# Kernel optimization log

Measured on AMD Instinct MI355X. Metric: run time of the kernel, lower is better.

## Reference

```python
import jax, jax.numpy as jnp
import numpy as np

B, N, M = 2, 1024, 512
D, H, DH = 1024, 16, 64          # features, heads, head dim (D == H*DH)
MID = H * DH
DC = 768                          # context_features
MULT = 4
EPS = 1e-5


def _ln(x, w, b):
    mu = jnp.mean(x, -1, keepdims=True)
    var = jnp.mean((x - mu) ** 2, -1, keepdims=True)
    return (x - mu) * jax.lax.rsqrt(var + EPS) * w + b


def _sincos(n, d):
    inv = 1.0 / (10000.0 ** (jnp.arange(0, d, 2, dtype=jnp.float32) / d))
    ang = jnp.arange(n, dtype=jnp.float32)[:, None] * inv[None, :]
    return jnp.sin(ang), jnp.cos(ang)


def _rope(x, sin, cos):
    # x: [B,H,N,DH]; sin/cos: [N, DH//2]; interleaved even/odd rotation
    s = sin[None, None]
    c = cos[None, None]
    xe = x[..., ::2]
    xo = x[..., 1::2]
    re = xe * c - xo * s
    ro = xe * s + xo * c
    return jnp.stack((re, ro), axis=-1).reshape(x.shape)


def _heads(t):
    b, n, _ = t.shape
    return t.reshape(b, n, H, DH).transpose(0, 2, 1, 3)


def _attn(xq, ctx, wq, wkv, wo, bo):
    q = _heads(xq @ wq)
    k, v = jnp.split(ctx @ wkv, 2, axis=-1)
    k = _heads(k)
    v = _heads(v)
    sq, cq = _sincos(q.shape[2], DH)
    sk, ck = _sincos(k.shape[2], DH)
    q = _rope(q, sq, cq)
    k = _rope(k, sk, ck)
    sim = jnp.einsum('bhnd,bhmd->bhnm', q, k) * (DH ** -0.5)
    a = jax.nn.softmax(sim, axis=-1)
    o = jnp.einsum('bhnm,bhmd->bhnd', a, v)
    o = o.transpose(0, 2, 1, 3).reshape(xq.shape[0], xq.shape[1], MID)
    return o @ wo + bo


def _adaln(x, c, lw, lb, gw, gb, bw, bb):
    g = (c @ gw + gb)[:, None, :]
    bt = (c @ bw + bb)[:, None, :]
    return _ln(x, lw, lb) * (1.0 + g) + bt


def setup_inputs() -> dict:
    ks = jax.random.split(jax.random.key(0), 24)
    s = 0.02
    inp = {
        'x': jax.random.normal(ks[0], (B, N, D), jnp.float32),
        'cond': jax.random.normal(ks[1], (B, D), jnp.float32),
        'context': jax.random.normal(ks[2], (B, M, DC), jnp.float32),
        # AdaLN (attn_mod) — reused for self- and cross-attention pre-norm
        'ln1_w': jnp.ones((D,), jnp.float32),
        'ln1_b': jnp.zeros((D,), jnp.float32),
        'g1_w': jax.random.normal(ks[3], (D, D), jnp.float32) * s,
        'g1_b': jnp.zeros((D,), jnp.float32),
        'b1_w': jax.random.normal(ks[4], (D, D), jnp.float32) * s,
        'b1_b': jnp.zeros((D,), jnp.float32),
        # AdaLN (ffn_mod)
        'ln2_w': jnp.ones((D,), jnp.float32),
        'ln2_b': jnp.zeros((D,), jnp.float32),
        'g2_w': jax.random.normal(ks[5], (D, D), jnp.float32) * s,
        'g2_b': jnp.zeros((D,), jnp.float32),
        'b2_w': jax.random.normal(ks[6], (D, D), jnp.float32) * s,
        'b2_b': jnp.zeros((D,), jnp.float32),
        # self-attention
        'sa_wq': jax.random.normal(ks[7], (D, MID), jnp.float32) * s,
        'sa_wkv': jax.random.normal(ks[8], (D, 2 * MID), jnp.float32) * s,
        'sa_wo': jax.random.normal(ks[9], (MID, D), jnp.float32) * s,
        'sa_bo': jnp.zeros((D,), jnp.float32),
        # cross-attention (context LayerNorm + projections)
        'ca_lnc_w': jnp.ones((DC,), jnp.float32),
        'ca_lnc_b': jnp.zeros((DC,), jnp.float32),
        'ca_wq': jax.random.normal(ks[10], (D, MID), jnp.float32) * s,
        'ca_wkv': jax.random.normal(ks[11], (DC, 2 * MID), jnp.float32) * s,
        'ca_wo': jax.random.normal(ks[12], (MID, D), jnp.float32) * s,
        'ca_bo': jnp.zeros((D,), jnp.float32),
        # FFN
        'ff_w1': jax.random.normal(ks[13], (D, MULT * D), jnp.float32) * s,
        'ff_b1': jnp.zeros((MULT * D,), jnp.float32),
        'ff_w2': jax.random.normal(ks[14], (MULT * D, D), jnp.float32) * s,
        'ff_b2': jnp.zeros((D,), jnp.float32),
    }
    return inp


def reference(x, cond, context,
              ln1_w, ln1_b, g1_w, g1_b, b1_w, b1_b,
              ln2_w, ln2_b, g2_w, g2_b, b2_w, b2_b,
              sa_wq, sa_wkv, sa_wo, sa_bo,
              ca_lnc_w, ca_lnc_b, ca_wq, ca_wkv, ca_wo, ca_bo,
              ff_w1, ff_b1, ff_w2, ff_b2):
    # self-attention with shared attn_mod AdaLN
    attn_in = _adaln(x, cond, ln1_w, ln1_b, g1_w, g1_b, b1_w, b1_b)
    x = _attn(attn_in, attn_in, sa_wq, sa_wkv, sa_wo, sa_bo) + x
    # cross-attention (attn_mod reused, context LayerNorm applied)
    cross_in = _adaln(x, cond, ln1_w, ln1_b, g1_w, g1_b, b1_w, b1_b)
    ctx_n = _ln(context, ca_lnc_w, ca_lnc_b)
    x = _attn(cross_in, ctx_n, ca_wq, ca_wkv, ca_wo, ca_bo) + x
    # FFN with ffn_mod AdaLN, exact GELU (torch default)
    ffn_in = _adaln(x, cond, ln2_w, ln2_b, g2_w, g2_b, b2_w, b2_b)
    h = jax.nn.gelu(ffn_in @ ff_w1 + ff_b1, approximate=False)
    x = h @ ff_w2 + ff_b2 + x
    return x
```

## Files before the change

kernel.cpp:

```cpp
#include <hip/hip_runtime.h>
#include <hip/hip_bf16.h>
#include <math.h>


typedef float f32x4 __attribute__((ext_vector_type(4)));
typedef __bf16 bf16x8 __attribute__((ext_vector_type(8)));
typedef __bf16 bf16x4 __attribute__((ext_vector_type(4)));
typedef __bf16 bf16x2 __attribute__((ext_vector_type(2)));

#define DEVI __device__ __forceinline__

DEVI void gload16(const void* g, void* l) {
  __builtin_amdgcn_global_load_lds((const __attribute__((address_space(1))) void*)g,
                                   (__attribute__((address_space(3))) void*)l, 16, 0, 0);
}

DEVI float fast_gelu(float x) {
  float a = fabsf(x) * 0.7071067811865475f;
  float tt = 1.0f / (1.0f + 0.3275911f * a);
  float p = tt * (0.254829592f + tt * (-0.284496736f + tt * (1.421413741f +
            tt * (-1.453152027f + tt * 1.061405429f))));
  float er = 1.0f - p * __expf(-a * a);
  er = (x < 0.f) ? -er : er;
  return 0.5f * x * (1.0f + er);
}

struct WtDesc {
  const float* src[8];
  __bf16* dst[8];
  int K[8], N[8];
  int tstart[9];
};

__global__ __launch_bounds__(256) void prep_kernel(WtDesc d,
                                                   float2* __restrict__ tbl,
                                                   const float* __restrict__ cond,
                                                   const float* __restrict__ g1w,
                                                   const float* __restrict__ b1w,
                                                   const float* __restrict__ g2w,
                                                   const float* __restrict__ b2w,
                                                   float* __restrict__ part) {
  __shared__ float smem[32 * 129];
  int blk = blockIdx.x;
  int wtend = d.tstart[8];
  int t = threadIdx.x;
  if (blk < wtend) {
    int e = 0;
#pragma unroll
    for (int i = 0; i < 7; ++i) e += (blk >= d.tstart[i + 1]) ? 1 : 0;
    int li = blk - d.tstart[e];
    const float* W = d.src[e];
    __bf16* WT = d.dst[e];
    int K = d.K[e], N = d.N[e];
    int ntx = N >> 7;
    int n0 = (li % ntx) * 128, k0 = (li / ntx) * 32;
    int tx = t & 31, ty = t >> 5;
#pragma unroll
    for (int i = 0; i < 4; ++i) {
      int k = ty + i * 8;
      f32x4 v = *(const f32x4*)(W + (size_t)(k0 + k) * N + n0 + tx * 4);
#pragma unroll
      for (int j = 0; j < 4; ++j) smem[k * 129 + tx * 4 + j] = v[j];
    }
    __syncthreads();
    int kc = t & 3;
#pragma unroll
    for (int i = 0; i < 2; ++i) {
      int n = i * 64 + (t >> 2);
      bf16x8 o;
#pragma unroll
      for (int j = 0; j < 8; ++j) o[j] = (__bf16)smem[(kc * 8 + j) * 129 + n];
      *(bf16x8*)(WT + (size_t)(n0 + n) * K + k0 + kc * 8) = o;
    }
  } else if (blk < wtend + 128) {
    int idx = (blk - wtend) * 256 + t;
    int n = idx >> 5, i = idx & 31;
    float inv = expf(-(float)(2 * i) * (1.0f / 64.0f) * 9.210340371976184f);
    float ang = (float)n * inv;
    tbl[idx] = make_float2(sinf(ang), cosf(ang));
  } else {
    int f = blk - wtend - 128;
    int dchunk = f & 3, b = (f >> 2) & 1, z = f >> 3;
    int mat = z >> 3, ks = z & 7;
    const float* W = (mat == 0) ? g1w : (mat == 1) ? b1w : (mat == 2) ? g2w : b2w;
    float* sc = smem;
    if (t < 128) sc[t] = cond[b * 1024 + ks * 128 + t];
    __syncthreads();
    int dd = dchunk * 256 + t;
    const float* Wp = W + (size_t)(ks * 128) * 1024 + dd;
    float acc = 0.f;
#pragma unroll 8
    for (int k = 0; k < 128; ++k) acc += sc[k] * Wp[(size_t)k * 1024];
    part[(size_t)(z * 2 + b) * 1024 + dd] = acc;
  }
}

__global__ __launch_bounds__(256) void mod_reduce_kernel(
    const float* __restrict__ part,
    const float* __restrict__ g1b, const float* __restrict__ b1b,
    const float* __restrict__ g2b, const float* __restrict__ b2b,
    float* __restrict__ mods) {
  int idx = blockIdx.x * 256 + threadIdx.x;
  int mat = idx >> 11, b = (idx >> 10) & 1, d = idx & 1023;
  float s = 0.f;
#pragma unroll
  for (int ks = 0; ks < 8; ++ks) s += part[(size_t)((mat * 8 + ks) * 2 + b) * 1024 + d];
  const float* Bv = (mat == 0) ? g1b : (mat == 1) ? b1b : (mat == 2) ? g2b : b2b;
  mods[(size_t)(mat * 2 + b) * 1024 + d] = s + Bv[d];
}

__global__ __launch_bounds__(256) void adaln_kernel(const float* __restrict__ X,
                                                    const float* __restrict__ lnw,
                                                    const float* __restrict__ lnb,
                                                    const float* __restrict__ mods,
                                                    int gi, int bi,
                                                    __bf16* __restrict__ out) {
  __shared__ float red[2][4];
  int row = blockIdx.x;
  int b = row >> 10;
  int t = threadIdx.x;
  const float4 xv = ((const float4*)(X + (size_t)row * 1024))[t];
  float s  = xv.x + xv.y + xv.z + xv.w;
  float s2 = xv.x * xv.x + xv.y * xv.y + xv.z * xv.z + xv.w * xv.w;
  int lane = t & 63, w = t >> 6;
#pragma unroll
  for (int off = 32; off > 0; off >>= 1) {
    s += __shfl_down(s, off);
    s2 += __shfl_down(s2, off);
  }
  if (lane == 0) { red[0][w] = s; red[1][w] = s2; }
  __syncthreads();
  s  = red[0][0] + red[0][1] + red[0][2] + red[0][3];
  s2 = red[1][0] + red[1][1] + red[1][2] + red[1][3];
  float mu = s * (1.0f / 1024.0f);
  float var = s2 * (1.0f / 1024.0f) - mu * mu;
  float rstd = rsqrtf(var + 1e-5f);
  const float4 wv = ((const float4*)lnw)[t];
  const float4 bv = ((const float4*)lnb)[t];
  const float4 gv = ((const float4*)(mods + (size_t)(gi * 2 + b) * 1024))[t];
  const float4 tv = ((const float4*)(mods + (size_t)(bi * 2 + b) * 1024))[t];
  bf16x4 ov;
  ov[0] = (__bf16)(((xv.x - mu) * rstd * wv.x + bv.x) * (1.0f + gv.x) + tv.x);
  ov[1] = (__bf16)(((xv.y - mu) * rstd * wv.y + bv.y) * (1.0f + gv.y) + tv.y);
  ov[2] = (__bf16)(((xv.z - mu) * rstd * wv.z + bv.z) * (1.0f + gv.z) + tv.z);
  ov[3] = (__bf16)(((xv.w - mu) * rstd * wv.w + bv.w) * (1.0f + gv.w) + tv.w);
  *(bf16x4*)(out + (size_t)row * 1024 + t * 4) = ov;
}

__global__ __launch_bounds__(256) void red_adaln_kernel(const float* __restrict__ part,
                                                        const float* __restrict__ bias,
                                                        const float* __restrict__ res,
                                                        const float* __restrict__ lnw,
                                                        const float* __restrict__ lnb,
                                                        const float* __restrict__ mods,
                                                        int gi, int bi, int MN,
                                                        float* __restrict__ xout,
                                                        __bf16* __restrict__ ain) {
  __shared__ float red[2][4];
  int row = blockIdx.x;
  int b = row >> 10;
  int t = threadIdx.x;
  size_t base = (size_t)row * 1024 + t * 4;
  float4 p0 = *(const float4*)(part + base);
  float4 p1 = *(const float4*)(part + MN + base);
  float4 rr = *(const float4*)(res + base);
  float4 bb = ((const float4*)bias)[t];
  float4 y;
  y.x = p0.x + p1.x + bb.x + rr.x;
  y.y = p0.y + p1.y + bb.y + rr.y;
  y.z = p0.z + p1.z + bb.z + rr.z;
  y.w = p0.w + p1.w + bb.w + rr.w;
  *(float4*)(xout + base) = y;
  float s  = y.x + y.y + y.z + y.w;
  float s2 = y.x * y.x + y.y * y.y + y.z * y.z + y.w * y.w;
  int lane = t & 63, w = t >> 6;
#pragma unroll
  for (int off = 32; off > 0; off >>= 1) {
    s += __shfl_down(s, off);
    s2 += __shfl_down(s2, off);
  }
  if (lane == 0) { red[0][w] = s; red[1][w] = s2; }
  __syncthreads();
  s  = red[0][0] + red[0][1] + red[0][2] + red[0][3];
  s2 = red[1][0] + red[1][1] + red[1][2] + red[1][3];
  float mu = s * (1.0f / 1024.0f);
  float var = s2 * (1.0f / 1024.0f) - mu * mu;
  float rstd = rsqrtf(var + 1e-5f);
  const float4 wv = ((const float4*)lnw)[t];
  const float4 bv = ((const float4*)lnb)[t];
  const float4 gv = ((const float4*)(mods + (size_t)(gi * 2 + b) * 1024))[t];
  const float4 tv = ((const float4*)(mods + (size_t)(bi * 2 + b) * 1024))[t];
  bf16x4 ov;
  ov[0] = (__bf16)(((y.x - mu) * rstd * wv.x + bv.x) * (1.0f + gv.x) + tv.x);
  ov[1] = (__bf16)(((y.y - mu) * rstd * wv.y + bv.y) * (1.0f + gv.y) + tv.y);
  ov[2] = (__bf16)(((y.z - mu) * rstd * wv.z + bv.z) * (1.0f + gv.z) + tv.z);
  ov[3] = (__bf16)(((y.w - mu) * rstd * wv.w + bv.w) * (1.0f + gv.w) + tv.w);
  *(bf16x4*)(ain + (size_t)row * 1024 + t * 4) = ov;
}

__global__ __launch_bounds__(256) void ctxln_kernel(const float* __restrict__ X,
                                                    const float* __restrict__ w,
                                                    const float* __restrict__ bias,
                                                    __bf16* __restrict__ out) {
  __shared__ float red[2][4];
  int row = blockIdx.x;
  int t = threadIdx.x;
  const float* xp = X + (size_t)row * 768;
  float v[3];
  float s = 0.f, s2 = 0.f;
#pragma unroll
  for (int i = 0; i < 3; ++i) {
    v[i] = xp[t + i * 256];
    s += v[i];
    s2 += v[i] * v[i];
  }
  int lane = t & 63, wv_ = t >> 6;
#pragma unroll
  for (int off = 32; off > 0; off >>= 1) {
    s += __shfl_down(s, off);
    s2 += __shfl_down(s2, off);
  }
  if (lane == 0) { red[0][wv_] = s; red[1][wv_] = s2; }
  __syncthreads();
  s  = red[0][0] + red[0][1] + red[0][2] + red[0][3];
  s2 = red[1][0] + red[1][1] + red[1][2] + red[1][3];
  float mu = s * (1.0f / 768.0f);
  float var = s2 * (1.0f / 768.0f) - mu * mu;
  float rstd = rsqrtf(var + 1e-5f);
#pragma unroll
  for (int i = 0; i < 3; ++i) {
    int c = t + i * 256;
    out[(size_t)row * 768 + c] = (__bf16)((v[i] - mu) * rstd * w[c] + bias[c]);
  }
}

__global__ __launch_bounds__(256) void vtb_kernel(const __bf16* __restrict__ Vb,
                                                  __bf16* __restrict__ VT, int Ntok) {
  __shared__ __bf16 tile[64][68];
  int bh = blockIdx.x, nt = blockIdx.y;
  int b = bh >> 4, h = bh & 15;
  int t = threadIdx.x;
  int tx = t & 15, ty = t >> 4;
#pragma unroll
  for (int i = 0; i < 4; ++i) {
    int n = ty + i * 16;
    bf16x4 v = *(const bf16x4*)(Vb + (size_t)(b * Ntok + nt * 64 + n) * 1024 + h * 64 + tx * 4);
#pragma unroll
    for (int j = 0; j < 4; ++j) tile[n][tx * 4 + j] = v[j];
  }
  __syncthreads();
#pragma unroll
  for (int i = 0; i < 4; ++i) {
    int d = ty + i * 16;
    bf16x4 o;
#pragma unroll
    for (int j = 0; j < 4; ++j) o[j] = tile[tx * 4 + j][d];
    *(bf16x4*)(VT + ((size_t)bh * 64 + d) * Ntok + nt * 64 + tx * 4) = o;
  }
}

template <int BM, int BN, int EPI, int DEPTH>
__global__ __launch_bounds__(256) void gemm3(const __bf16* __restrict__ A,
                                             const __bf16* __restrict__ BT,
                                             const float* __restrict__ bias,
                                             const float* __restrict__ res,
                                             void* __restrict__ outv,
                                             int M, int N, int K, int kslices,
                                             const float2* __restrict__ tbl,
                                             __bf16* __restrict__ Qro,
                                             __bf16* __restrict__ Kro,
                                             __bf16* __restrict__ Vbo,
                                             int Ntok) {
  constexpr int MI = BM / 32, NI = BN / 32;
  constexpr int NBUF = DEPTH + 1;
  constexpr int LPT = BM / 64 + BN / 64;
  __shared__ __bf16 sA[NBUF][BM * 32];
  __shared__ __bf16 sB[NBUF][BN * 32];
  const int t = threadIdx.x;
  const int w = t >> 6, lane = t & 63;
  const int lr = lane & 15, lg = lane >> 4;
  const int fxor = (lr >> 1) & 3;
  int nwg = gridDim.x * gridDim.y * gridDim.z;
  int flat = blockIdx.x + gridDim.x * (blockIdx.y + gridDim.y * blockIdx.z);
  flat = (flat & 7) * (nwg >> 3) + (flat >> 3);
  const int bn = flat % gridDim.y;
  int rest = flat / gridDim.y;
  const int bm = rest % gridDim.x;
  const int bz = rest / gridDim.x;
  const int wm = (w >> 1) * (BM / 2), wn = (w & 1) * (BN / 2);
  const int kper = K / kslices;
  const int k0 = bz * kper;
  const int nsteps = kper / 32;
  f32x4 acc[MI][NI] = {};

  auto stage = [&](int buf, int kt) {
#pragma unroll
    for (int i = 0; i < BM / 64; ++i) {
      int e8 = i * 256 + t;
      int row = e8 >> 2, c = e8 & 3;
      int scol = (c ^ ((row >> 1) & 3)) << 3;
      gload16(A + (size_t)(bm * BM + row) * K + kt + scol, &sA[buf][e8 * 8]);
    }
#pragma unroll
    for (int i = 0; i < BN / 64; ++i) {
      int e8 = i * 256 + t;
      int row = e8 >> 2, c = e8 & 3;
      int scol = (c ^ ((row >> 1) & 3)) << 3;
      gload16(BT + (size_t)(bn * BN + row) * K + kt + scol, &sB[buf][e8 * 8]);
    }
  };

  auto compute = [&](int buf) {
    bf16x8 af[MI], bfr[NI];
#pragma unroll
    for (int mi = 0; mi < MI; ++mi)
      af[mi] = *(const bf16x8*)(&sA[buf][(wm + mi * 16 + lr) * 32 + ((lg ^ fxor) << 3)]);
#pragma unroll
    for (int ni = 0; ni < NI; ++ni)
      bfr[ni] = *(const bf16x8*)(&sB[buf][(wn + ni * 16 + lr) * 32 + ((lg ^ fxor) << 3)]);
    __builtin_amdgcn_s_setprio(1);
#pragma unroll
    for (int mi = 0; mi < MI; ++mi)
#pragma unroll
      for (int ni = 0; ni < NI; ++ni)
        acc[mi][ni] = __builtin_amdgcn_mfma_f32_16x16x32_bf16(af[mi], bfr[ni], acc[mi][ni], 0, 0, 0);
    __builtin_amdgcn_s_setprio(0);
  };

#pragma unroll
  for (int i = 0; i < DEPTH; ++i) stage(i, k0 + i * 32);

  int it = 0;
  for (; it < nsteps - (DEPTH - 1); ++it) {
    asm volatile("s_waitcnt vmcnt(%0)" :: "n"((DEPTH - 1) * LPT) : "memory");
    __builtin_amdgcn_s_barrier();
    __builtin_amdgcn_sched_barrier(0);
    if (it + DEPTH < nsteps) stage((it + DEPTH) % NBUF, k0 + (it + DEPTH) * 32);
    compute(it % NBUF);
  }
  asm volatile("s_waitcnt vmcnt(0)" ::: "memory");
  __builtin_amdgcn_s_barrier();
  __builtin_amdgcn_sched_barrier(0);
  for (; it < nsteps; ++it) compute(it % NBUF);

#pragma unroll
  for (int mi = 0; mi < MI; ++mi) {
    int row = bm * BM + wm + mi * 16 + lg * 4;
#pragma unroll
    for (int ni = 0; ni < NI; ++ni) {
      int col = bn * BN + wn + ni * 16 + lr;
#pragma unroll
      for (int r = 0; r < 4; ++r) {
        float v = acc[mi][ni][r];
        int erow = row + r;
        size_t off = (size_t)erow * N + col;
        if (EPI == 0) {
          ((float*)outv)[off] = v;
        } else if (EPI == 1) {
          ((float*)outv)[off] = v + bias[col] + res[off];
        } else if (EPI == 2) {
          ((__bf16*)outv)[off] = (__bf16)fast_gelu(v + bias[col]);
        } else if (EPI == 3) {
          ((float*)outv)[(size_t)bz * M * N + off] = v;
        } else if (EPI == 4) {
          float ov = __shfl_xor(v, 1);
          int b = erow >> 10, n = erow & 1023;
          if (col < 2048) {
            int h = (col >> 6) & 15, dh = col & 63;
            float2 sc = tbl[n * 32 + (dh >> 1)];
            float rv = (lr & 1) ? (ov * sc.x + v * sc.y) : (v * sc.y - ov * sc.x);
            __bf16* dst;
            if (col < 1024) { rv *= 0.125f; dst = Qro; } else dst = Kro;
            dst[((size_t)(b * 16 + h) * Ntok + n) * 64 + dh] = (__bf16)rv;
          } else {
            Vbo[(size_t)erow * 1024 + (col - 2048)] = (__bf16)v;
          }
        }
      }
    }
  }
}

__global__ __launch_bounds__(256) void gemm_cross(const __bf16* __restrict__ Aq,
                                                  const __bf16* __restrict__ Bq,
                                                  const __bf16* __restrict__ Akv,
                                                  const __bf16* __restrict__ Bkv,
                                                  const float2* __restrict__ tbl,
                                                  __bf16* __restrict__ Qro,
                                                  __bf16* __restrict__ Kro,
                                                  __bf16* __restrict__ Vbo) {
  constexpr int BM = 128, BN = 64, DEPTH = 3, NBUF = 4, LPT = 3;
  constexpr int MI = 4, NI = 2;
  __shared__ __bf16 sA[NBUF][BM * 32];
  __shared__ __bf16 sB[NBUF][BN * 32];
  const int t = threadIdx.x;
  const int w = t >> 6, lane = t & 63;
  const int lr = lane & 15, lg = lane >> 4;
  const int fxor = (lr >> 1) & 3;
  int flat = blockIdx.x;
  flat = (flat & 7) * 64 + (flat >> 3);
  const bool isq = flat < 256;
  const __bf16* A  = isq ? Aq : Akv;
  const __bf16* BT = isq ? Bq : Bkv;
  const int K = isq ? 1024 : 768;
  int lf = isq ? flat : flat - 256;
  const int bn = isq ? (lf & 15) : (lf & 31);
  const int bm = isq ? (lf >> 4) : (lf >> 5);
  const int wm = (w >> 1) * 64, wn = (w & 1) * 32;
  const int nsteps = K >> 5;
  f32x4 acc[MI][NI] = {};

  auto stage = [&](int buf, int kt) {
#pragma unroll
    for (int i = 0; i < 2; ++i) {
      int e8 = i * 256 + t;
      int row = e8 >> 2, c = e8 & 3;
      int scol = (c ^ ((row >> 1) & 3)) << 3;
      gload16(A + (size_t)(bm * BM + row) * K + kt + scol, &sA[buf][e8 * 8]);
    }
    {
      int e8 = t;
      int row = e8 >> 2, c = e8 & 3;
      int scol = (c ^ ((row >> 1) & 3)) << 3;
      gload16(BT + (size_t)(bn * BN + row) * K + kt + scol, &sB[buf][e8 * 8]);
    }
  };

  auto compute = [&](int buf) {
    bf16x8 af[MI], bfr[NI];
#pragma unroll
    for (int mi = 0; mi < MI; ++mi)
      af[mi] = *(const bf16x8*)(&sA[buf][(wm + mi * 16 + lr) * 32 + ((lg ^ fxor) << 3)]);
#pragma unroll
    for (int ni = 0; ni < NI; ++ni)
      bfr[ni] = *(const bf16x8*)(&sB[buf][(wn + ni * 16 + lr) * 32 + ((lg ^ fxor) << 3)]);
    __builtin_amdgcn_s_setprio(1);
#pragma unroll
    for (int mi = 0; mi < MI; ++mi)
#pragma unroll
      for (int ni = 0; ni < NI; ++ni)
        acc[mi][ni] = __builtin_amdgcn_mfma_f32_16x16x32_bf16(af[mi], bfr[ni], acc[mi][ni], 0, 0, 0);
    __builtin_amdgcn_s_setprio(0);
  };

#pragma unroll
  for (int i = 0; i < DEPTH; ++i) stage(i, i * 32);

  int it = 0;
  for (; it < nsteps - (DEPTH - 1); ++it) {
    asm volatile("s_waitcnt vmcnt(%0)" :: "n"((DEPTH - 1) * LPT) : "memory");
    __builtin_amdgcn_s_barrier();
    __builtin_amdgcn_sched_barrier(0);
    if (it + DEPTH < nsteps) stage((it + DEPTH) % NBUF, (it + DEPTH) * 32);
    compute(it % NBUF);
  }
  asm volatile("s_waitcnt vmcnt(0)" ::: "memory");
  __builtin_amdgcn_s_barrier();
  __builtin_amdgcn_sched_barrier(0);
  for (; it < nsteps; ++it) compute(it % NBUF);

#pragma unroll
  for (int mi = 0; mi < MI; ++mi) {
    int row = bm * 128 + wm + mi * 16 + lg * 4;
#pragma unroll
    for (int ni = 0; ni < NI; ++ni) {
      int col = bn * 64 + wn + ni * 16 + lr;
#pragma unroll
      for (int r = 0; r < 4; ++r) {
        float v = acc[mi][ni][r];
        int erow = row + r;
        float ov = __shfl_xor(v, 1);
        if (isq) {
          int b = erow >> 10, n = erow & 1023;
          int h = col >> 6, dh = col & 63;
          float2 sc = tbl[n * 32 + (dh >> 1)];
          float rv = ((lr & 1) ? (ov * sc.x + v * sc.y) : (v * sc.y - ov * sc.x)) * 0.125f;
          Qro[((size_t)(b * 16 + h) * 1024 + n) * 64 + dh] = (__bf16)rv;
        } else {
          int b = erow >> 9, n = erow & 511;
          if (col < 1024) {
            int h = col >> 6, dh = col & 63;
            float2 sc = tbl[n * 32 + (dh >> 1)];
            float rv = (lr & 1) ? (ov * sc.x + v * sc.y) : (v * sc.y - ov * sc.x);
            Kro[((size_t)(b * 16 + h) * 512 + n) * 64 + dh] = (__bf16)rv;
          } else {
            Vbo[(size_t)erow * 1024 + (col - 1024)] = (__bf16)v;
          }
        }
      }
    }
  }
}

__global__ __launch_bounds__(256) void ff2red_kernel(const float* __restrict__ part,
                                                     const float* __restrict__ bias,
                                                     const float* __restrict__ res,
                                                     float* __restrict__ out, int MN, int N) {
  int idx = blockIdx.x * 256 + threadIdx.x;
  float4 p0 = ((const float4*)part)[idx];
  float4 p1 = ((const float4*)(part + MN))[idx];
  float4 rr = ((const float4*)res)[idx];
  int colb = (idx * 4) & (N - 1);
  float4 bb = *(const float4*)(bias + colb);
  float4 o;
  o.x = p0.x + p1.x + bb.x + rr.x;
  o.y = p0.y + p1.y + bb.y + rr.y;
  o.z = p0.z + p1.z + bb.z + rr.z;
  o.w = p0.w + p1.w + bb.w + rr.w;
  ((float4*)out)[idx] = o;
}

template <int KITERS>
__global__ __launch_bounds__(256) void attn_kernel(const __bf16* __restrict__ Qr,
                                                   const __bf16* __restrict__ Kr,
                                                   const __bf16* __restrict__ VT,
                                                   __bf16* __restrict__ O,
                                                   int Nq, int Nk) {
  __shared__ __bf16 sK[2][64 * 64];
  __shared__ __bf16 sV[2][64 * 64];
  __shared__ __bf16 Pl[4][16 * 64];
  const int t = threadIdx.x, w = t >> 6, lane = t & 63;
  const int lr = lane & 15, lg = lane >> 4;
  const int lsrc = lane & 48;
  const int swz = (lr & 7) << 3;
  int flat = blockIdx.x + (blockIdx.y << 4);
  flat = (flat & 7) * 64 + (flat >> 3);
  const int bh = flat >> 4;
  const int q0 = (flat & 15) * 64 + w * 16;
  const int b = bh >> 4, h = bh & 15;

  auto stage = [&](int buf, int kt) {
#pragma unroll
    for (int i = 0; i < 2; ++i) {
      int e8 = i * 256 + t;
      int row = e8 >> 3, col8 = e8 & 7;
      int scol = (col8 ^ (row & 7)) << 3;
      gload16(Kr + ((size_t)bh * Nk + kt + row) * 64 + scol, &sK[buf][e8 * 8]);
      gload16(VT + ((size_t)bh * 64 + row) * Nk + kt + scol, &sV[buf][e8 * 8]);
    }
  };

  bf16x8 qf[2];
#pragma unroll
  for (int kh = 0; kh < 2; ++kh)
    qf[kh] = *(const bf16x8*)(Qr + ((size_t)bh * Nq + q0 + lr) * 64 + kh * 32 + lg * 8);
  f32x4 accO[4] = {};
  float m = -INFINITY, l = 0.f;

  stage(0, 0);
  __syncthreads();
  int cur = 0;
#pragma unroll
  for (int it = 0; it < KITERS; ++it) {
    if (it + 1 < KITERS) stage(cur ^ 1, (it + 1) * 64);
    f32x4 s[4] = {};
    __builtin_amdgcn_s_setprio(1);
#pragma unroll
    for (int nf = 0; nf < 4; ++nf) {
      int r = nf * 16 + lr;
#pragma unroll
      for (int kh = 0; kh < 2; ++kh) {
        bf16x8 kf = *(const bf16x8*)(&sK[cur][r * 64 + (((kh * 4 + lg) ^ (lr & 7)) << 3)]);
        s[nf] = __builtin_amdgcn_mfma_f32_16x16x32_bf16(kf, qf[kh], s[nf], 0, 0, 0);
      }
    }
    __builtin_amdgcn_s_setprio(0);
    float p[16];
#pragma unroll
    for (int j = 0; j < 16; ++j) p[j] = s[j >> 2][j & 3];
    float pm = p[0];
#pragma unroll
    for (int j = 1; j < 16; ++j) pm = fmaxf(pm, p[j]);
    pm = fmaxf(pm, __shfl_xor(pm, 16));
    pm = fmaxf(pm, __shfl_xor(pm, 32));
    if (!__all(pm <= m + 8.f)) {
      float mnew = fmaxf(m, pm);
      float resc = __expf(m - mnew);
      float rq[4];
#pragma unroll
      for (int r = 0; r < 4; ++r) rq[r] = __shfl(resc, lsrc | (lg * 4 + r));
#pragma unroll
      for (int df = 0; df < 4; ++df)
#pragma unroll
        for (int r = 0; r < 4; ++r) accO[df][r] *= rq[r];
      l *= resc;
      m = mnew;
    }
    float rs = 0.f;
#pragma unroll
    for (int j = 0; j < 16; ++j) { p[j] = __expf(p[j] - m); rs += p[j]; }
    rs += __shfl_xor(rs, 16);
    rs += __shfl_xor(rs, 32);
    l += rs;
#pragma unroll
    for (int nf = 0; nf < 4; ++nf)
#pragma unroll
      for (int jj = 0; jj < 2; ++jj) {
        int k = nf * 16 + lg * 4 + 2 * jj;
        bf16x2 pk;
        pk[0] = (__bf16)p[nf * 4 + 2 * jj];
        pk[1] = (__bf16)p[nf * 4 + 2 * jj + 1];
        *(bf16x2*)(&Pl[w][lr * 64 + (k ^ swz)]) = pk;
      }
    bf16x8 pa0 = *(const bf16x8*)(&Pl[w][lr * 64 + ((lg * 8) ^ swz)]);
    bf16x8 pa1 = *(const bf16x8*)(&Pl[w][lr * 64 + ((32 + lg * 8) ^ swz)]);
    __builtin_amdgcn_s_setprio(1);
#pragma unroll
    for (int df = 0; df < 4; ++df) {
      int d = df * 16 + lr;
      bf16x8 vf0 = *(const bf16x8*)(&sV[cur][d * 64 + ((lg ^ (lr & 7)) << 3)]);
      bf16x8 vf1 = *(const bf16x8*)(&sV[cur][d * 64 + (((4 + lg) ^ (lr & 7)) << 3)]);
      accO[df] = __builtin_amdgcn_mfma_f32_16x16x32_bf16(pa0, vf0, accO[df], 0, 0, 0);
      accO[df] = __builtin_amdgcn_mfma_f32_16x16x32_bf16(pa1, vf1, accO[df], 0, 0, 0);
    }
    __builtin_amdgcn_s_setprio(0);
    __syncthreads();
    cur ^= 1;
  }
  float lq[4];
#pragma unroll
  for (int r = 0; r < 4; ++r) lq[r] = __shfl(l, lsrc | (lg * 4 + r));
#pragma unroll
  for (int r = 0; r < 4; ++r) {
    float inv = 1.0f / lq[r];
    int n = q0 + lg * 4 + r;
#pragma unroll
    for (int df = 0; df < 4; ++df)
      O[(size_t)(b * 1024 + n) * 1024 + h * 64 + df * 16 + lr] = (__bf16)(accO[df][r] * inv);
  }
}

extern "C" void kernel_launch(void* const* d_in, const int* in_sizes, int n_in,
                              void* d_out, int out_size, void* d_ws, size_t ws_size,
                              hipStream_t stream) {
  (void)in_sizes; (void)n_in; (void)out_size; (void)ws_size;
  const float* x       = (const float*)d_in[0];
  const float* cond    = (const float*)d_in[1];
  const float* ctx     = (const float*)d_in[2];
  const float* ln1_w   = (const float*)d_in[3];
  const float* ln1_b   = (const float*)d_in[4];
  const float* g1_w    = (const float*)d_in[5];
  const float* g1_b    = (const float*)d_in[6];
  const float* b1_w    = (const float*)d_in[7];
  const float* b1_b    = (const float*)d_in[8];
  const float* ln2_w   = (const float*)d_in[9];
  const float* ln2_b   = (const float*)d_in[10];
  const float* g2_w    = (const float*)d_in[11];
  const float* g2_b    = (const float*)d_in[12];
  const float* b2_w    = (const float*)d_in[13];
  const float* b2_b    = (const float*)d_in[14];
  const float* sa_wq   = (const float*)d_in[15];
  const float* sa_wkv  = (const float*)d_in[16];
  const float* sa_wo   = (const float*)d_in[17];
  const float* sa_bo   = (const float*)d_in[18];
  const float* ca_lnc_w = (const float*)d_in[19];
  const float* ca_lnc_b = (const float*)d_in[20];
  const float* ca_wq   = (const float*)d_in[21];
  const float* ca_wkv  = (const float*)d_in[22];
  const float* ca_wo   = (const float*)d_in[23];
  const float* ca_bo   = (const float*)d_in[24];
  const float* ff_w1   = (const float*)d_in[25];
  const float* ff_b1   = (const float*)d_in[26];
  const float* ff_w2   = (const float*)d_in[27];
  const float* ff_b2   = (const float*)d_in[28];
  float* out = (float*)d_out;

  char* ws = (char*)d_ws;
  size_t o = 0;
  auto alloc = [&](size_t bytes) {
    void* p = ws + o;
    o += (bytes + 255) & ~(size_t)255;
    return p;
  };

  __bf16* wqT   = (__bf16*)alloc(1024ull * 1024 * 2);
  __bf16* wkvT  = (__bf16*)alloc(2048ull * 1024 * 2);
  __bf16* woT   = (__bf16*)alloc(1024ull * 1024 * 2);
  __bf16* cwqT  = (__bf16*)alloc(1024ull * 1024 * 2);
  __bf16* cwkvT = (__bf16*)alloc(2048ull * 768 * 2);
  __bf16* cwoT  = (__bf16*)alloc(1024ull * 1024 * 2);
  __bf16* ff1T  = (__bf16*)alloc(4096ull * 1024 * 2);
  __bf16* ff2T  = (__bf16*)alloc(1024ull * 4096 * 2);
  float*  mods  = (float*)alloc(4ull * 2 * 1024 * 4);
  float2* tbl   = (float2*)alloc(1024ull * 32 * 8);
  __bf16* ain   = (__bf16*)alloc(2048ull * 1024 * 2);
  float*  Qf    = (float*)alloc(2048ull * 1024 * 4);
  float*  KVf   = (float*)alloc(2048ull * 2048 * 4);
  __bf16* ctxn  = (__bf16*)alloc(1024ull * 768 * 2);
  __bf16* Qr    = (__bf16*)alloc(2048ull * 1024 * 2);
  __bf16* Kr    = (__bf16*)alloc(2048ull * 1024 * 2);
  __bf16* VTb   = (__bf16*)alloc(2048ull * 1024 * 2);
  __bf16* Ob    = (__bf16*)alloc(2048ull * 1024 * 2);
  float*  x1    = (float*)alloc(2048ull * 1024 * 4);
  float*  x2    = (float*)alloc(2048ull * 1024 * 4);
  __bf16* hb    = (__bf16*)KVf;
  float*  pbuf  = (float*)Qr;
  float*  wopb  = (float*)KVf;
  float*  mpart = (float*)Qf;
  __bf16* Vb    = (__bf16*)Qf;

  WtDesc wd;
  const float* srcs[8] = {sa_wq, sa_wkv, sa_wo, ca_wq, ca_wkv, ca_wo, ff_w1, ff_w2};
  __bf16* dsts[8] = {wqT, wkvT, woT, cwqT, cwkvT, cwoT, ff1T, ff2T};
  int Ks[8] = {1024, 1024, 1024, 1024, 768, 1024, 1024, 4096};
  int Ns[8] = {1024, 2048, 1024, 1024, 2048, 1024, 4096, 1024};
  int cum = 0;
  for (int i = 0; i < 8; ++i) {
    wd.src[i] = srcs[i]; wd.dst[i] = dsts[i]; wd.K[i] = Ks[i]; wd.N[i] = Ns[i];
    wd.tstart[i] = cum;
    cum += (Ks[i] >> 5) * (Ns[i] >> 7);
  }
  wd.tstart[8] = cum;
  prep_kernel<<<cum + 128 + 256, 256, 0, stream>>>(wd, tbl, cond, g1_w, b1_w, g2_w, b2_w, mpart);
  mod_reduce_kernel<<<32, 256, 0, stream>>>(mpart, g1_b, b1_b, g2_b, b2_b, mods);

  adaln_kernel<<<2048, 256, 0, stream>>>(x, ln1_w, ln1_b, mods, 0, 1, ain);
  gemm3<128, 64, 4, 3><<<dim3(16, 48), 256, 0, stream>>>(ain, wqT, nullptr, nullptr, nullptr,
                                                         2048, 3072, 1024, 1, tbl, Qr, Kr, Vb, 1024);
  vtb_kernel<<<dim3(32, 16), 256, 0, stream>>>(Vb, VTb, 1024);
  attn_kernel<16><<<dim3(16, 32), 256, 0, stream>>>(Qr, Kr, VTb, Ob, 1024, 1024);
  gemm3<128, 64, 3, 3><<<dim3(16, 16, 2), 256, 0, stream>>>(Ob, woT, nullptr, nullptr, wopb,
                                                            2048, 1024, 1024, 2, nullptr, nullptr, nullptr, nullptr, 0);
  red_adaln_kernel<<<2048, 256, 0, stream>>>(wopb, sa_bo, x, ln1_w, ln1_b, mods, 0, 1,
                                             2048 * 1024, x1, ain);

  ctxln_kernel<<<1024, 256, 0, stream>>>(ctx, ca_lnc_w, ca_lnc_b, ctxn);
  gemm_cross<<<512, 256, 0, stream>>>(ain, cwqT, ctxn, cwkvT, tbl, Qr, Kr, Vb);
  vtb_kernel<<<dim3(32, 8), 256, 0, stream>>>(Vb, VTb, 512);
  attn_kernel<8><<<dim3(16, 32), 256, 0, stream>>>(Qr, Kr, VTb, Ob, 1024, 512);
  gemm3<128, 64, 3, 3><<<dim3(16, 16, 2), 256, 0, stream>>>(Ob, cwoT, nullptr, nullptr, wopb,
                                                            2048, 1024, 1024, 2, nullptr, nullptr, nullptr, nullptr, 0);
  red_adaln_kernel<<<2048, 256, 0, stream>>>(wopb, ca_bo, x1, ln2_w, ln2_b, mods, 2, 3,
                                             2048 * 1024, x2, ain);

  gemm3<128, 128, 2, 2><<<dim3(16, 32), 256, 0, stream>>>(ain, ff1T, ff_b1, nullptr, hb,
                                                          2048, 4096, 1024, 1, nullptr, nullptr, nullptr, nullptr, 0);
  gemm3<128, 64, 3, 3><<<dim3(16, 16, 2), 256, 0, stream>>>(hb, ff2T, nullptr, nullptr, pbuf,
                                                            2048, 1024, 4096, 2, nullptr, nullptr, nullptr, nullptr, 0);
  ff2red_kernel<<<2048, 256, 0, stream>>>(pbuf, ff_b2, x2, out, 2048 * 1024, 1024);
}
```

Baseline: 241.4 us.

## Replace 4-wave GEMM with single-wave 64x64 tile kernel without barriers

The templated 256-thread GEMM, which used 128x64 or 128x128 block tiles, is replaced by a 64-thread single-wavefront kernel that computes a 64x64 tile. With one wave per block, the LDS staging needs no s_barrier, so the barriers are removed and the kernel relies only on vmcnt waits. Grids grow to many more small blocks. The aim is to drop barrier stalls and raise occupancy. The cost is less tile reuse per block, so more global and L2 traffic per FLOP.

New measurement: 295.2 us. +22.3%, slower.

```diff
diff --git a/kernel.cpp b/kernel.cpp
--- a/kernel.cpp
+++ b/kernel.cpp
@@ -259,8 +259,8 @@
   }
 }
 
-template <int BM, int BN, int EPI, int DEPTH>
-__global__ __launch_bounds__(256) void gemm3(const __bf16* __restrict__ A,
+template <int EPI, int DEPTH>
+__global__ __launch_bounds__(64) void gemm1w(const __bf16* __restrict__ A,
                                              const __bf16* __restrict__ BT,
                                              const float* __restrict__ bias,
                                              const float* __restrict__ res,
@@ -271,14 +271,12 @@
                                              __bf16* __restrict__ Kro,
                                              __bf16* __restrict__ Vbo,
                                              int Ntok) {
-  constexpr int MI = BM / 32, NI = BN / 32;
   constexpr int NBUF = DEPTH + 1;
-  constexpr int LPT = BM / 64 + BN / 64;
-  __shared__ __bf16 sA[NBUF][BM * 32];
-  __shared__ __bf16 sB[NBUF][BN * 32];
+  constexpr int LPT = 8;
+  __shared__ __bf16 sA[NBUF][64 * 32];
+  __shared__ __bf16 sB[NBUF][64 * 32];
   const int t = threadIdx.x;
-  const int w = t >> 6, lane = t & 63;
-  const int lr = lane & 15, lg = lane >> 4;
+  const int lr = t & 15, lg = t >> 4;
   const int fxor = (lr >> 1) & 3;
   int nwg = gridDim.x * gridDim.y * gridDim.z;
   int flat = blockIdx.x + gridDim.x * (blockIdx.y + gridDim.y * blockIdx.z);
@@ -287,42 +285,41 @@
   int rest = flat / gridDim.y;
   const int bm = rest % gridDim.x;
   const int bz = rest / gridDim.x;
-  const int wm = (w >> 1) * (BM / 2), wn = (w & 1) * (BN / 2);
   const int kper = K / kslices;
   const int k0 = bz * kper;
   const int nsteps = kper / 32;
-  f32x4 acc[MI][NI] = {};
+  f32x4 acc[4][4] = {};
 
   auto stage = [&](int buf, int kt) {
 #pragma unroll
-    for (int i = 0; i < BM / 64; ++i) {
-      int e8 = i * 256 + t;
+    for (int i = 0; i < 4; ++i) {
+      int e8 = i * 64 + t;
       int row = e8 >> 2, c = e8 & 3;
       int scol = (c ^ ((row >> 1) & 3)) << 3;
-      gload16(A + (size_t)(bm * BM + row) * K + kt + scol, &sA[buf][e8 * 8]);
-    }
-#pragma unroll
-    for (int i = 0; i < BN / 64; ++i) {
-      int e8 = i * 256 + t;
+      gload16(A + (size_t)(bm * 64 + row) * K + kt + scol, &sA[buf][e8 * 8]);
+    }
+#pragma unroll
+    for (int i = 0; i < 4; ++i) {
+      int e8 = i * 64 + t;
       int row = e8 >> 2, c = e8 & 3;
       int scol = (c ^ ((row >> 1) & 3)) << 3;
-      gload16(BT + (size_t)(bn * BN + row) * K + kt + scol, &sB[buf][e8 * 8]);
+      gload16(BT + (size_t)(bn * 64 + row) * K + kt + scol, &sB[buf][e8 * 8]);
     }
   };
 
   auto compute = [&](int buf) {
-    bf16x8 af[MI], bfr[NI];
-#pragma unroll
-    for (int mi = 0; mi < MI; ++mi)
-      af[mi] = *(const bf16x8*)(&sA[buf][(wm + mi * 16 + lr) * 32 + ((lg ^ fxor) << 3)]);
-#pragma unroll
-    for (int ni = 0; ni < NI; ++ni)
-      bfr[ni] = *(const bf16x8*)(&sB[buf][(wn + ni * 16 + lr) * 32 + ((lg ^ fxor) << 3)]);
+    bf16x8 af[4], bfr[4];
+#pragma unroll
+    for (int mi = 0; mi < 4; ++mi)
+      af[mi] = *(const bf16x8*)(&sA[buf][(mi * 16 + lr) * 32 + ((lg ^ fxor) << 3)]);
+#pragma unroll
+    for (int ni = 0; ni < 4; ++ni)
+      bfr[ni] = *(const bf16x8*)(&sB[buf][(ni * 16 + lr) * 32 + ((lg ^ fxor) << 3)]);
     __builtin_amdgcn_s_setprio(1);
 #pragma unroll
-    for (int mi = 0; mi < MI; ++mi)
-#pragma unroll
-      for (int ni = 0; ni < NI; ++ni)
+    for (int mi = 0; mi < 4; ++mi)
+#pragma unroll
+      for (int ni = 0; ni < 4; ++ni)
         acc[mi][ni] = __builtin_amdgcn_mfma_f32_16x16x32_bf16(af[mi], bfr[ni], acc[mi][ni], 0, 0, 0);
     __builtin_amdgcn_s_setprio(0);
   };
@@ -333,22 +330,20 @@
   int it = 0;
   for (; it < nsteps - (DEPTH - 1); ++it) {
     asm volatile("s_waitcnt vmcnt(%0)" :: "n"((DEPTH - 1) * LPT) : "memory");
-    __builtin_amdgcn_s_barrier();
     __builtin_amdgcn_sched_barrier(0);
     if (it + DEPTH < nsteps) stage((it + DEPTH) % NBUF, k0 + (it + DEPTH) * 32);
     compute(it % NBUF);
   }
   asm volatile("s_waitcnt vmcnt(0)" ::: "memory");
-  __builtin_amdgcn_s_barrier();
   __builtin_amdgcn_sched_barrier(0);
   for (; it < nsteps; ++it) compute(it % NBUF);
 
 #pragma unroll
-  for (int mi = 0; mi < MI; ++mi) {
-    int row = bm * BM + wm + mi * 16 + lg * 4;
-#pragma unroll
-    for (int ni = 0; ni < NI; ++ni) {
-      int col = bn * BN + wn + ni * 16 + lr;
+  for (int mi = 0; mi < 4; ++mi) {
+    int row = bm * 64 + mi * 16 + lg * 4;
+#pragma unroll
+    for (int ni = 0; ni < 4; ++ni) {
+      int col = bn * 64 + ni * 16 + lr;
 #pragma unroll
       for (int r = 0; r < 4; ++r) {
         float v = acc[mi][ni][r];
@@ -715,12 +710,12 @@
   mod_reduce_kernel<<<32, 256, 0, stream>>>(mpart, g1_b, b1_b, g2_b, b2_b, mods);
 
   adaln_kernel<<<2048, 256, 0, stream>>>(x, ln1_w, ln1_b, mods, 0, 1, ain);
-  gemm3<128, 64, 4, 3><<<dim3(16, 48), 256, 0, stream>>>(ain, wqT, nullptr, nullptr, nullptr,
-                                                         2048, 3072, 1024, 1, tbl, Qr, Kr, Vb, 1024);
+  gemm1w<4, 3><<<dim3(32, 48), 64, 0, stream>>>(ain, wqT, nullptr, nullptr, nullptr,
+                                                2048, 3072, 1024, 1, tbl, Qr, Kr, Vb, 1024);
   vtb_kernel<<<dim3(32, 16), 256, 0, stream>>>(Vb, VTb, 1024);
   attn_kernel<16><<<dim3(16, 32), 256, 0, stream>>>(Qr, Kr, VTb, Ob, 1024, 1024);
-  gemm3<128, 64, 3, 3><<<dim3(16, 16, 2), 256, 0, stream>>>(Ob, woT, nullptr, nullptr, wopb,
-                                                            2048, 1024, 1024, 2, nullptr, nullptr, nullptr, nullptr, 0);
+  gemm1w<3, 3><<<dim3(32, 16, 2), 64, 0, stream>>>(Ob, woT, nullptr, nullptr, wopb,
+                                                   2048, 1024, 1024, 2, nullptr, nullptr, nullptr, nullptr, 0);
   red_adaln_kernel<<<2048, 256, 0, stream>>>(wopb, sa_bo, x, ln1_w, ln1_b, mods, 0, 1,
                                              2048 * 1024, x1, ain);
 
@@ -728,14 +723,14 @@
   gemm_cross<<<512, 256, 0, stream>>>(ain, cwqT, ctxn, cwkvT, tbl, Qr, Kr, Vb);
   vtb_kernel<<<dim3(32, 8), 256, 0, stream>>>(Vb, VTb, 512);
   attn_kernel<8><<<dim3(16, 32), 256, 0, stream>>>(Qr, Kr, VTb, Ob, 1024, 512);
-  gemm3<128, 64, 3, 3><<<dim3(16, 16, 2), 256, 0, stream>>>(Ob, cwoT, nullptr, nullptr, wopb,
-                                                            2048, 1024, 1024, 2, nullptr, nullptr, nullptr, nullptr, 0);
+  gemm1w<3, 3><<<dim3(32, 16, 2), 64, 0, stream>>>(Ob, cwoT, nullptr, nullptr, wopb,
+                                                   2048, 1024, 1024, 2, nullptr, nullptr, nullptr, nullptr, 0);
   red_adaln_kernel<<<2048, 256, 0, stream>>>(wopb, ca_bo, x1, ln2_w, ln2_b, mods, 2, 3,
                                              2048 * 1024, x2, ain);
 
-  gemm3<128, 128, 2, 2><<<dim3(16, 32), 256, 0, stream>>>(ain, ff1T, ff_b1, nullptr, hb,
-                                                          2048, 4096, 1024, 1, nullptr, nullptr, nullptr, nullptr, 0);
-  gemm3<128, 64, 3, 3><<<dim3(16, 16, 2), 256, 0, stream>>>(hb, ff2T, nullptr, nullptr, pbuf,
-                                                            2048, 1024, 4096, 2, nullptr, nullptr, nullptr, nullptr, 0);
+  gemm1w<2, 3><<<dim3(32, 64), 64, 0, stream>>>(ain, ff1T, ff_b1, nullptr, hb,
+                                                2048, 4096, 1024, 1, nullptr, nullptr, nullptr, nullptr, 0);
+  gemm1w<3, 3><<<dim3(32, 16, 2), 64, 0, stream>>>(hb, ff2T, nullptr, nullptr, pbuf,
+                                                   2048, 1024, 4096, 2, nullptr, nullptr, nullptr, nullptr, 0);
   ff2red_kernel<<<2048, 256, 0, stream>>>(pbuf, ff_b2, x2, out, 2048 * 1024, 1024);
 }
```
